# Kernel tuning notes

Hardware: AMD Instinct MI355X
Metric: run time of the kernel (lower is better)

The kernel has to match this reference:

```python
import jax, jax.numpy as jnp
import numpy as np

B, C, D, H, W = 4, 128, 16, 16, 16
INNER = 64  # channels // reduction


def setup_inputs() -> dict:
    key = jax.random.key(0)
    ks = jax.random.split(key, 4)
    s = 0.02
    return {
        "x": jax.random.normal(ks[0], (B, C, D, H, W), dtype=jnp.float32),
        "Wq": jax.random.normal(ks[1], (INNER, C), dtype=jnp.float32) * s,
        "bq": jnp.zeros((INNER,), dtype=jnp.float32),
        "Wk": jax.random.normal(ks[2], (INNER, C), dtype=jnp.float32) * s,
        "bk": jnp.zeros((INNER,), dtype=jnp.float32),
        "Wv": jax.random.normal(ks[3], (C, C), dtype=jnp.float32) * s,
        "bv": jnp.zeros((C,), dtype=jnp.float32),
        "gamma": jnp.zeros((1,), dtype=jnp.float32),
    }


def reference(x, Wq, bq, Wk, bk, Wv, bv, gamma):
    b, c, d, h, w = x.shape
    n = d * h * w
    inner = Wq.shape[0]
    scale = inner ** (-0.5)
    xf = x.reshape(b, c, n)  # flatten spatial dims
    # 1x1 Conv3d == per-position channel matmul
    q = jnp.einsum('oc,bcn->bon', Wq, xf) + bq[None, :, None]  # [B, inner, N]
    k = jnp.einsum('oc,bcn->bon', Wk, xf) + bk[None, :, None]  # [B, inner, N]
    v = jnp.einsum('oc,bcn->bon', Wv, xf) + bv[None, :, None]  # [B, C, N]
    # attn[b, n, m] = softmax_m(q[:, :, n] . k[:, :, m] * scale)
    attn = jax.nn.softmax(jnp.einsum('bon,bom->bnm', q, k) * scale, axis=-1)
    # out = v @ attn^T  -> out[b, c, n] = sum_m v[b, c, m] * attn[b, n, m]
    out = jnp.einsum('bcm,bnm->bcn', v, attn).reshape(b, c, d, h, w)
    return x + gamma[0] * out
```

## Files before the change

kernel.cpp:

```cpp
#include <hip/hip_runtime.h>
#include <cstdint>

#define B_ 4
#define C_ 128
#define INNER_ 64
#define N_ 4096
#define S_ 8
#define KEYS_PER_BLOCK (N_ / S_)
#define KT 64
#define NT (KEYS_PER_BLOCK / KT)

typedef __attribute__((ext_vector_type(8))) short short8;
typedef __attribute__((ext_vector_type(4))) short bf16x4;
typedef __attribute__((ext_vector_type(4))) float f32x4;

typedef const __attribute__((address_space(1))) void* gp_t;
typedef __attribute__((address_space(3))) void* lp_t;

__device__ __forceinline__ short f2bf(float f) {
  unsigned u = __builtin_bit_cast(unsigned, f);
  unsigned r = (u + 0x7FFFu + ((u >> 16) & 1u)) >> 16;
  return (short)r;
}
__device__ __forceinline__ float bf2f(short s) {
  return __builtin_bit_cast(float, ((unsigned)(unsigned short)s) << 16);
}

__device__ __forceinline__ f32x4 mfma16(bf16x4 a, bf16x4 b, f32x4 c) {
#if __has_builtin(__builtin_amdgcn_mfma_f32_16x16x16bf16_1k)
  return __builtin_amdgcn_mfma_f32_16x16x16bf16_1k(a, b, c, 0, 0, 0);
#elif __has_builtin(__builtin_amdgcn_mfma_f32_16x16x16_bf16)
  return __builtin_amdgcn_mfma_f32_16x16x16_bf16(a, b, c, 0, 0, 0);
#else
  f32x4 d;
  asm volatile("v_mfma_f32_16x16x16_bf16 %0, %1, %2, %3"
               : "=v"(d) : "v"(a), "v"(b), "v"(c));
  return d;
#endif
}

__global__ __launch_bounds__(256) void pack_kernel(
    const float* __restrict__ Wq, const float* __restrict__ bq,
    const float* __restrict__ Wk, const float* __restrict__ bk,
    const float* __restrict__ Wv, const float* __restrict__ bv,
    short* __restrict__ wp, float* __restrict__ bp)
{
  const int idx = blockIdx.x * 256 + threadIdx.x;
  const int o = idx >> 7, c = idx & 127;
  float v;
  if (o < 64)       v = Wq[o * C_ + c];
  else if (o < 128) v = Wk[(o - 64) * C_ + c];
  else              v = Wv[(o - 128) * C_ + c];
  wp[idx] = f2bf(v);
  if (c == 0)
    bp[o] = (o < 64) ? bq[o] : (o < 128) ? bk[o - 64] : bv[o - 128];
}

__global__ __launch_bounds__(256) void qkv_kernel(
    const float* __restrict__ x, const short* __restrict__ wp,
    const float* __restrict__ bp,
    short* __restrict__ qg, short* __restrict__ kg, short* __restrict__ vg)
{
  __shared__ short xT[32 * 136];
  __shared__ short outb[256 * 40];
  __shared__ float biasL[256];

  const int tid = threadIdx.x;
  const int b   = blockIdx.x >> 7;
  const int n0  = (blockIdx.x & 127) << 5;

  biasL[tid] = bp[tid];
  const float* xb = x + (size_t)b * C_ * N_ + n0;
  for (int i = tid; i < 1024; i += 256) {
    const int c = i >> 3, seg = i & 7;
    const float4 v = *(const float4*)&xb[(size_t)c * N_ + seg * 4];
    xT[(seg * 4 + 0) * 136 + c] = f2bf(v.x);
    xT[(seg * 4 + 1) * 136 + c] = f2bf(v.y);
    xT[(seg * 4 + 2) * 136 + c] = f2bf(v.z);
    xT[(seg * 4 + 3) * 136 + c] = f2bf(v.w);
  }
  __syncthreads();

  const int w = tid >> 6, lane = tid & 63, quad = lane >> 4, l16 = lane & 15;

  short8 xf[2][4];
#pragma unroll
  for (int nt = 0; nt < 2; ++nt)
#pragma unroll
    for (int kk = 0; kk < 4; ++kk)
      xf[nt][kk] = *(const short8*)&xT[(nt * 16 + l16) * 136 + kk * 32 + quad * 8];

  if (w < 2) {
    const int obase = w * 64;
#pragma unroll
    for (int ot = 0; ot < 4; ++ot) {
      const int o = obase + ot * 16 + l16;
      short8 wf[4];
#pragma unroll
      for (int kk = 0; kk < 4; ++kk)
        wf[kk] = *(const short8*)&wp[(size_t)o * 128 + kk * 32 + quad * 8];
      const float bias = biasL[o];
#pragma unroll
      for (int nt = 0; nt < 2; ++nt) {
        f32x4 acc = (f32x4){0.f, 0.f, 0.f, 0.f};
#pragma unroll
        for (int kk = 0; kk < 4; ++kk)
          acc = __builtin_amdgcn_mfma_f32_16x16x32_bf16(xf[nt][kk], wf[kk], acc, 0, 0, 0);
#pragma unroll
        for (int r = 0; r < 4; ++r)
          outb[o * 40 + nt * 16 + quad * 4 + r] = f2bf(acc[r] + bias);
      }
    }
  } else {
    const int ob2 = (w - 2) * 64;
#pragma unroll
    for (int ot = 0; ot < 4; ++ot) {
      const int orow = 128 + ob2 + ot * 16 + l16;
      short8 wf[4];
#pragma unroll
      for (int kk = 0; kk < 4; ++kk)
        wf[kk] = *(const short8*)&wp[(size_t)orow * 128 + kk * 32 + quad * 8];
#pragma unroll
      for (int nt = 0; nt < 2; ++nt) {
        f32x4 acc = (f32x4){0.f, 0.f, 0.f, 0.f};
#pragma unroll
        for (int kk = 0; kk < 4; ++kk)
          acc = __builtin_amdgcn_mfma_f32_16x16x32_bf16(wf[kk], xf[nt][kk], acc, 0, 0, 0);
#pragma unroll
        for (int r = 0; r < 4; ++r) {
          const int o_r = 128 + ob2 + ot * 16 + quad * 4 + r;
          outb[o_r * 40 + nt * 16 + l16] = f2bf(acc[r] + biasL[o_r]);
        }
      }
    }
  }
  __syncthreads();

  {
    const int n = tid >> 3, oc = tid & 7;
    short8 qv, kv;
#pragma unroll
    for (int j = 0; j < 8; ++j) {
      qv[j] = outb[(oc * 8 + j) * 40 + n];
      kv[j] = outb[(64 + oc * 8 + j) * 40 + n];
    }
    *(short8*)&qg[(((size_t)b * N_ + n0 + n) << 6) + oc * 8] = qv;
    *(short8*)&kg[(((size_t)b * N_ + n0 + n) << 6) + oc * 8] = kv;
#pragma unroll
    for (int rep = 0; rep < 2; ++rep) {
      const int idx2 = tid + rep * 256;
      const int orel = idx2 >> 2, nc = idx2 & 3;
      const short8 vv = *(const short8*)&outb[(128 + orel) * 40 + nc * 8];
      *(short8*)&vg[(((size_t)b * C_ + orel) << 12) + n0 + nc * 8] = vv;
    }
  }
}

__global__ __launch_bounds__(256, 3) void attn_kernel(
    const short* __restrict__ qb, const short* __restrict__ kb,
    const short* __restrict__ vb,
    short* __restrict__ Opart, float* __restrict__ lbuf)
{
  __shared__ short kbuf[2][4096];
  __shared__ short vbuf[2][8192];

  const int tid = threadIdx.x;
  const int bid = blockIdx.x;
  const int b   = bid >> 8;
  const int qt  = (bid >> 3) & 31;
  const int s   = bid & 7;
  const int m0  = qt << 7;
  const int w   = tid >> 6, lane = tid & 63, quad = lane >> 4, l16 = lane & 15;
  const int rbase = m0 + w * 32;

  const float kS = 0.125f * 1.44269504088896340736f;

  short8 qa[2][2];
#pragma unroll
  for (int mt = 0; mt < 2; ++mt)
#pragma unroll
    for (int kk = 0; kk < 2; ++kk)
      qa[mt][kk] = *(const short8*)&qb[((size_t)b * N_ + rbase + mt * 16 + l16) * 64 + kk * 32 + quad * 8];

  float lsum[2] = {0.f, 0.f};
  f32x4 accO[8][2];
#pragma unroll
  for (int vt = 0; vt < 8; ++vt)
#pragma unroll
    for (int mt = 0; mt < 2; ++mt) accO[vt][mt] = (f32x4){0.f, 0.f, 0.f, 0.f};

  const int kslice = s * KEYS_PER_BLOCK;

  auto dma_tile = [&](int kt, int d) {
    const int kbase = kslice + kt * KT;
#pragma unroll
    for (int t = 0; t < 2; ++t) {
      const int p = (w * 2 + t) * 64 + lane;
      const int key = p >> 3, jm = (p & 7) ^ (key & 7);
      const short* src = kb + (((size_t)b * N_ + kbase + key) << 6) + jm * 8;
      __builtin_amdgcn_global_load_lds((gp_t)src, (lp_t)&kbuf[d][(w * 2 + t) * 512], 16, 0, 0);
    }
#pragma unroll
    for (int t = 0; t < 4; ++t) {
      const int p = (w * 4 + t) * 64 + lane;
      const int ch = p >> 3, jm = (p & 7) ^ (ch & 7);
      const short* src = vb + ((size_t)b * C_ + ch) * N_ + kbase + jm * 8;
      __builtin_amdgcn_global_load_lds((gp_t)src, (lp_t)&vbuf[d][(w * 4 + t) * 512], 16, 0, 0);
    }
  };

  dma_tile(0, 0);

  for (int kt = 0; kt < NT; ++kt) {
    __syncthreads();
    if (kt + 1 < NT) dma_tile(kt + 1, (kt + 1) & 1);
    const int d = kt & 1;

    bf16x4 pbf[4][2];
#pragma unroll
    for (int ct = 0; ct < 4; ++ct) {
      const short8 kf0 = *(const short8*)&kbuf[d][((ct * 16 + l16) << 6) + ((quad ^ (l16 & 7)) << 3)];
      const short8 kf1 = *(const short8*)&kbuf[d][((ct * 16 + l16) << 6) + (((4 + quad) ^ (l16 & 7)) << 3)];
#pragma unroll
      for (int mt = 0; mt < 2; ++mt) {
        f32x4 st = (f32x4){0.f, 0.f, 0.f, 0.f};
        st = __builtin_amdgcn_mfma_f32_16x16x32_bf16(kf0, qa[mt][0], st, 0, 0, 0);
        st = __builtin_amdgcn_mfma_f32_16x16x32_bf16(kf1, qa[mt][1], st, 0, 0, 0);
        bf16x4 p4;
#pragma unroll
        for (int r = 0; r < 4; ++r) {
          const float p = exp2f(st[r] * kS);
          lsum[mt] += p;
          p4[r] = f2bf(p);
        }
        pbf[ct][mt] = p4;
      }
    }

#pragma unroll
    for (int vt = 0; vt < 8; ++vt) {
#pragma unroll
      for (int ct = 0; ct < 4; ++ct) {
        const int chunk = ct * 2 + (quad >> 1);
        const bf16x4 vf = *(const bf16x4*)&vbuf[d][((vt * 16 + l16) << 6) +
                              ((chunk ^ (l16 & 7)) << 3) + ((quad & 1) << 2)];
        accO[vt][0] = mfma16(vf, pbf[ct][0], accO[vt][0]);
        accO[vt][1] = mfma16(vf, pbf[ct][1], accO[vt][1]);
      }
    }
  }

#pragma unroll
  for (int mt = 0; mt < 2; ++mt) {
    lsum[mt] += __shfl_xor(lsum[mt], 16);
    lsum[mt] += __shfl_xor(lsum[mt], 32);
  }
  if (quad == 0) {
#pragma unroll
    for (int mt = 0; mt < 2; ++mt)
      lbuf[((size_t)b * S_ + s) * N_ + rbase + mt * 16 + l16] = lsum[mt];
  }
#pragma unroll
  for (int vt = 0; vt < 8; ++vt) {
#pragma unroll
    for (int mt = 0; mt < 2; ++mt) {
#pragma unroll
      for (int r = 0; r < 4; ++r) {
        const int ch = vt * 16 + quad * 4 + r;
        Opart[(((size_t)b * S_ + s) * C_ + ch) * N_ + rbase + mt * 16 + l16] =
            f2bf(accO[vt][mt][r]);
      }
    }
  }
}

__global__ __launch_bounds__(256) void linv_kernel(
    const float* __restrict__ lbuf, float* __restrict__ linv)
{
  const int idx = blockIdx.x * 256 + threadIdx.x;
  const int b = idx >> 12, n = idx & (N_ - 1);
  float L = 0.f;
#pragma unroll
  for (int s = 0; s < S_; ++s) L += lbuf[((size_t)b * S_ + s) * N_ + n];
  linv[idx] = 1.f / L;
}

__global__ __launch_bounds__(256) void combine_kernel(
    const float* __restrict__ x, const float* __restrict__ gamma,
    const short* __restrict__ Opart, const float* __restrict__ linv,
    float* __restrict__ out)
{
  const int idx = blockIdx.x * 256 + threadIdx.x;
  const int n = (idx & 511) << 3;
  const int c = (idx >> 9) & 127;
  const int b = idx >> 16;

  float acc[8];
#pragma unroll
  for (int j = 0; j < 8; ++j) acc[j] = 0.f;
#pragma unroll
  for (int s = 0; s < S_; ++s) {
    const short8 o8 = *(const short8*)&Opart[(((size_t)b * S_ + s) * C_ + c) * N_ + n];
#pragma unroll
    for (int j = 0; j < 8; ++j) acc[j] += bf2f(o8[j]);
  }
  const float4 li0 = *(const float4*)&linv[((size_t)b << 12) + n];
  const float4 li1 = *(const float4*)&linv[((size_t)b << 12) + n + 4];
  const float g = gamma[0];
  const size_t xi = ((size_t)b * C_ + c) * N_ + n;
  const float4 x0 = *(const float4*)&x[xi];
  const float4 x1 = *(const float4*)&x[xi + 4];
  float4 o0, o1;
  o0.x = x0.x + g * acc[0] * li0.x;  o0.y = x0.y + g * acc[1] * li0.y;
  o0.z = x0.z + g * acc[2] * li0.z;  o0.w = x0.w + g * acc[3] * li0.w;
  o1.x = x1.x + g * acc[4] * li1.x;  o1.y = x1.y + g * acc[5] * li1.y;
  o1.z = x1.z + g * acc[6] * li1.z;  o1.w = x1.w + g * acc[7] * li1.w;
  *(float4*)&out[xi] = o0;
  *(float4*)&out[xi + 4] = o1;
}

extern "C" void kernel_launch(void* const* d_in, const int* in_sizes, int n_in,
                              void* d_out, int out_size, void* d_ws, size_t ws_size,
                              hipStream_t stream) {
  const float* x     = (const float*)d_in[0];
  const float* Wq    = (const float*)d_in[1];
  const float* bq    = (const float*)d_in[2];
  const float* Wk    = (const float*)d_in[3];
  const float* bk    = (const float*)d_in[4];
  const float* Wv    = (const float*)d_in[5];
  const float* bv    = (const float*)d_in[6];
  const float* gamma = (const float*)d_in[7];
  float* out = (float*)d_out;

  short* qb = (short*)d_ws;
  short* kb = qb + (size_t)B_ * N_ * INNER_;
  short* vb = kb + (size_t)B_ * N_ * INNER_;
  short* Opart = vb + (size_t)B_ * C_ * N_;
  float* lbuf  = (float*)(Opart + (size_t)B_ * S_ * C_ * N_);
  float* linv  = lbuf + (size_t)B_ * S_ * N_;
  float* bp    = linv + (size_t)B_ * N_;
  short* wp    = (short*)(bp + 256);

  pack_kernel<<<128, 256, 0, stream>>>(Wq, bq, Wk, bk, Wv, bv, wp, bp);
  qkv_kernel<<<B_ * (N_ / 32), 256, 0, stream>>>(x, wp, bp, qb, kb, vb);
  attn_kernel<<<B_ * (N_ / 128) * S_, 256, 0, stream>>>(qb, kb, vb, Opart, lbuf);
  linv_kernel<<<(B_ * N_) / 256, 256, 0, stream>>>(lbuf, linv);
  combine_kernel<<<(B_ * C_ * N_ / 8) / 256, 256, 0, stream>>>(x, gamma, Opart, linv, out);
}
```

Measured before the change: 134.9 us.

## Halve attention key tile to raise occupancy and use packed bf16 conversion

Shrinks the key tile from 64 to 32 keys. This halves the shared K/V double buffers and raises the launch-bounds occupancy hint from 3 to 4 blocks per CU. The V swizzle and DMA mapping are reworked for the narrower tile, and the P-times-V loop order is changed. Probabilities are converted to bf16 with a packed hardware conversion when one is available. The trade-off is twice as many barrier-separated iterations, with less latency hiding per iteration.

```diff
diff --git a/kernel.cpp b/kernel.cpp
--- a/kernel.cpp
+++ b/kernel.cpp
@@ -7,12 +7,13 @@
 #define N_ 4096
 #define S_ 8
 #define KEYS_PER_BLOCK (N_ / S_)
-#define KT 64
+#define KT 32
 #define NT (KEYS_PER_BLOCK / KT)
 
 typedef __attribute__((ext_vector_type(8))) short short8;
 typedef __attribute__((ext_vector_type(4))) short bf16x4;
 typedef __attribute__((ext_vector_type(4))) float f32x4;
+typedef __attribute__((ext_vector_type(2))) unsigned u32x2;
 
 typedef const __attribute__((address_space(1))) void* gp_t;
 typedef __attribute__((address_space(3))) void* lp_t;
@@ -24,6 +25,15 @@
 }
 __device__ __forceinline__ float bf2f(short s) {
   return __builtin_bit_cast(float, ((unsigned)(unsigned short)s) << 16);
+}
+__device__ __forceinline__ unsigned pk2(float lo, float hi) {
+#if __has_builtin(__builtin_amdgcn_cvt_pk_bf16_f32)
+  typedef __attribute__((ext_vector_type(2))) __bf16 bfp;
+  bfp v = __builtin_amdgcn_cvt_pk_bf16_f32(lo, hi);
+  return __builtin_bit_cast(unsigned, v);
+#else
+  return (unsigned)(unsigned short)f2bf(lo) | ((unsigned)(unsigned short)f2bf(hi) << 16);
+#endif
 }
 
 __device__ __forceinline__ f32x4 mfma16(bf16x4 a, bf16x4 b, f32x4 c) {
@@ -156,13 +166,13 @@
   }
 }
 
-__global__ __launch_bounds__(256, 3) void attn_kernel(
+__global__ __launch_bounds__(256, 4) void attn_kernel(
     const short* __restrict__ qb, const short* __restrict__ kb,
     const short* __restrict__ vb,
     short* __restrict__ Opart, float* __restrict__ lbuf)
 {
-  __shared__ short kbuf[2][4096];
-  __shared__ short vbuf[2][8192];
+  __shared__ short kbuf[2][2048];
+  __shared__ short vbuf[2][4096];
 
   const int tid = threadIdx.x;
   const int bid = blockIdx.x;
@@ -193,19 +203,18 @@
 
   auto dma_tile = [&](int kt, int d) {
     const int kbase = kslice + kt * KT;
+    {
+      const int p = w * 64 + lane;
+      const int key = p >> 3, jm = (p & 7) ^ (key & 7);
+      const short* src = kb + (((size_t)b * N_ + kbase + key) << 6) + jm * 8;
+      __builtin_amdgcn_global_load_lds((gp_t)src, (lp_t)&kbuf[d][w * 512], 16, 0, 0);
+    }
 #pragma unroll
     for (int t = 0; t < 2; ++t) {
       const int p = (w * 2 + t) * 64 + lane;
-      const int key = p >> 3, jm = (p & 7) ^ (key & 7);
-      const short* src = kb + (((size_t)b * N_ + kbase + key) << 6) + jm * 8;
-      __builtin_amdgcn_global_load_lds((gp_t)src, (lp_t)&kbuf[d][(w * 2 + t) * 512], 16, 0, 0);
-    }
-#pragma unroll
-    for (int t = 0; t < 4; ++t) {
-      const int p = (w * 4 + t) * 64 + lane;
-      const int ch = p >> 3, jm = (p & 7) ^ (ch & 7);
+      const int ch = p >> 2, jm = (p & 3) ^ (ch & 3);
       const short* src = vb + ((size_t)b * C_ + ch) * N_ + kbase + jm * 8;
-      __builtin_amdgcn_global_load_lds((gp_t)src, (lp_t)&vbuf[d][(w * 4 + t) * 512], 16, 0, 0);
+      __builtin_amdgcn_global_load_lds((gp_t)src, (lp_t)&vbuf[d][(w * 2 + t) * 512], 16, 0, 0);
     }
   };
 
@@ -216,9 +225,9 @@
     if (kt + 1 < NT) dma_tile(kt + 1, (kt + 1) & 1);
     const int d = kt & 1;
 
-    bf16x4 pbf[4][2];
-#pragma unroll
-    for (int ct = 0; ct < 4; ++ct) {
+    bf16x4 pbf[2][2];
+#pragma unroll
+    for (int ct = 0; ct < 2; ++ct) {
       const short8 kf0 = *(const short8*)&kbuf[d][((ct * 16 + l16) << 6) + ((quad ^ (l16 & 7)) << 3)];
       const short8 kf1 = *(const short8*)&kbuf[d][((ct * 16 + l16) << 6) + (((4 + quad) ^ (l16 & 7)) << 3)];
 #pragma unroll
@@ -226,26 +235,26 @@
         f32x4 st = (f32x4){0.f, 0.f, 0.f, 0.f};
         st = __builtin_amdgcn_mfma_f32_16x16x32_bf16(kf0, qa[mt][0], st, 0, 0, 0);
         st = __builtin_amdgcn_mfma_f32_16x16x32_bf16(kf1, qa[mt][1], st, 0, 0, 0);
-        bf16x4 p4;
-#pragma unroll
-        for (int r = 0; r < 4; ++r) {
-          const float p = exp2f(st[r] * kS);
-          lsum[mt] += p;
-          p4[r] = f2bf(p);
-        }
-        pbf[ct][mt] = p4;
-      }
-    }
-
-#pragma unroll
-    for (int vt = 0; vt < 8; ++vt) {
-#pragma unroll
-      for (int ct = 0; ct < 4; ++ct) {
-        const int chunk = ct * 2 + (quad >> 1);
-        const bf16x4 vf = *(const bf16x4*)&vbuf[d][((vt * 16 + l16) << 6) +
-                              ((chunk ^ (l16 & 7)) << 3) + ((quad & 1) << 2)];
-        accO[vt][0] = mfma16(vf, pbf[ct][0], accO[vt][0]);
-        accO[vt][1] = mfma16(vf, pbf[ct][1], accO[vt][1]);
+        const float p0 = exp2f(st[0] * kS);
+        const float p1 = exp2f(st[1] * kS);
+        const float p2 = exp2f(st[2] * kS);
+        const float p3 = exp2f(st[3] * kS);
+        lsum[mt] += (p0 + p1) + (p2 + p3);
+        u32x2 pp;
+        pp[0] = pk2(p0, p1);
+        pp[1] = pk2(p2, p3);
+        pbf[ct][mt] = __builtin_bit_cast(bf16x4, pp);
+      }
+    }
+
+#pragma unroll
+    for (int ks = 0; ks < 2; ++ks) {
+#pragma unroll
+      for (int vt = 0; vt < 8; ++vt) {
+        const bf16x4 vf = *(const bf16x4*)&vbuf[d][((vt * 16 + l16) << 5) +
+                              ((((ks * 2 + (quad >> 1)) ^ (l16 & 3))) << 3) + ((quad & 1) << 2)];
+        accO[vt][0] = mfma16(vf, pbf[ks][0], accO[vt][0]);
+        accO[vt][1] = mfma16(vf, pbf[ks][1], accO[vt][1]);
       }
     }
   }
```

Result: slower. 140.5 us (+4.2%).

## Retile V into MFMA-ready key tiles, rebalance splits, fuse linv into combine

Applied to the files above, without the earlier changes.

The qkv kernel now writes V in a tiled layout (per 64-key tile, grouped in 4-key chunks across channels), so each attention tile DMA is one contiguous copy and V fragments are read from LDS with simple strided loads and no swizzle. The key dimension is split 6 ways instead of 8, giving uneven tile counts per split, which cuts grid size to 768 blocks and shrinks the partial-output buffer. The linv kernel is folded into combine, which computes the reciprocal row sums in shared memory per 64-column block. Softmax probabilities are packed with a paired bf16 convert. The uneven splits create some load imbalance, and the new combine launches fewer blocks, each doing more work.

```diff
diff --git a/kernel.cpp b/kernel.cpp
--- a/kernel.cpp
+++ b/kernel.cpp
@@ -5,14 +5,13 @@
 #define C_ 128
 #define INNER_ 64
 #define N_ 4096
-#define S_ 8
-#define KEYS_PER_BLOCK (N_ / S_)
+#define SPLITS 6
 #define KT 64
-#define NT (KEYS_PER_BLOCK / KT)
 
 typedef __attribute__((ext_vector_type(8))) short short8;
 typedef __attribute__((ext_vector_type(4))) short bf16x4;
 typedef __attribute__((ext_vector_type(4))) float f32x4;
+typedef __attribute__((ext_vector_type(2))) unsigned u32x2;
 
 typedef const __attribute__((address_space(1))) void* gp_t;
 typedef __attribute__((address_space(3))) void* lp_t;
@@ -24,6 +23,15 @@
 }
 __device__ __forceinline__ float bf2f(short s) {
   return __builtin_bit_cast(float, ((unsigned)(unsigned short)s) << 16);
+}
+__device__ __forceinline__ unsigned pk2(float lo, float hi) {
+#if __has_builtin(__builtin_amdgcn_cvt_pk_bf16_f32)
+  typedef __attribute__((ext_vector_type(2))) __bf16 bfp;
+  bfp v = __builtin_amdgcn_cvt_pk_bf16_f32(lo, hi);
+  return __builtin_bit_cast(unsigned, v);
+#else
+  return (unsigned)(unsigned short)f2bf(lo) | ((unsigned)(unsigned short)f2bf(hi) << 16);
+#endif
 }
 
 __device__ __forceinline__ f32x4 mfma16(bf16x4 a, bf16x4 b, f32x4 c) {
@@ -146,12 +154,22 @@
     }
     *(short8*)&qg[(((size_t)b * N_ + n0 + n) << 6) + oc * 8] = qv;
     *(short8*)&kg[(((size_t)b * N_ + n0 + n) << 6) + oc * 8] = kv;
+  }
+  {
+    const int T = n0 >> 6;
+    const int k4base = (n0 & 63) >> 2;
 #pragma unroll
     for (int rep = 0; rep < 2; ++rep) {
-      const int idx2 = tid + rep * 256;
-      const int orel = idx2 >> 2, nc = idx2 & 3;
-      const short8 vv = *(const short8*)&outb[(128 + orel) * 40 + nc * 8];
-      *(short8*)&vg[(((size_t)b * C_ + orel) << 12) + n0 + nc * 8] = vv;
+      const int idx2 = rep * 256 + tid;
+      const int c0  = idx2 & 63;
+      const int k4l = idx2 >> 6;
+      const bf16x4 lo = *(const bf16x4*)&outb[(128 + 2 * c0) * 40 + k4l * 4];
+      const bf16x4 hi = *(const bf16x4*)&outb[(128 + 2 * c0 + 1) * 40 + k4l * 4];
+      short8 vv;
+#pragma unroll
+      for (int j = 0; j < 4; ++j) { vv[j] = lo[j]; vv[4 + j] = hi[j]; }
+      const size_t tb = (((size_t)b * 64 + T) * 16 + k4base + k4l) * 512 + c0 * 8;
+      *(short8*)&vg[tb] = vv;
     }
   }
 }
@@ -166,13 +184,16 @@
 
   const int tid = threadIdx.x;
   const int bid = blockIdx.x;
-  const int b   = bid >> 8;
-  const int qt  = (bid >> 3) & 31;
-  const int s   = bid & 7;
+  const int s   = bid % 6;
+  const int qt  = (bid / 6) & 31;
+  const int b   = bid / 192;
   const int m0  = qt << 7;
   const int w   = tid >> 6, lane = tid & 63, quad = lane >> 4, l16 = lane & 15;
   const int rbase = m0 + w * 32;
 
+  const int t0  = (s * 64) / 6;
+  const int NTs = ((s + 1) * 64) / 6 - t0;
+
   const float kS = 0.125f * 1.44269504088896340736f;
 
   short8 qa[2][2];
@@ -189,31 +210,29 @@
 #pragma unroll
     for (int mt = 0; mt < 2; ++mt) accO[vt][mt] = (f32x4){0.f, 0.f, 0.f, 0.f};
 
-  const int kslice = s * KEYS_PER_BLOCK;
-
   auto dma_tile = [&](int kt, int d) {
-    const int kbase = kslice + kt * KT;
+    const int T = t0 + kt;
+    const short* kbp = kb + (((size_t)b * N_ + T * 64) << 6);
 #pragma unroll
     for (int t = 0; t < 2; ++t) {
       const int p = (w * 2 + t) * 64 + lane;
       const int key = p >> 3, jm = (p & 7) ^ (key & 7);
-      const short* src = kb + (((size_t)b * N_ + kbase + key) << 6) + jm * 8;
+      const short* src = kbp + (key << 6) + jm * 8;
       __builtin_amdgcn_global_load_lds((gp_t)src, (lp_t)&kbuf[d][(w * 2 + t) * 512], 16, 0, 0);
     }
+    const short* vtp = vb + ((size_t)b * 64 + T) * 8192;
 #pragma unroll
     for (int t = 0; t < 4; ++t) {
       const int p = (w * 4 + t) * 64 + lane;
-      const int ch = p >> 3, jm = (p & 7) ^ (ch & 7);
-      const short* src = vb + ((size_t)b * C_ + ch) * N_ + kbase + jm * 8;
-      __builtin_amdgcn_global_load_lds((gp_t)src, (lp_t)&vbuf[d][(w * 4 + t) * 512], 16, 0, 0);
+      __builtin_amdgcn_global_load_lds((gp_t)(vtp + p * 8), (lp_t)&vbuf[d][(w * 4 + t) * 512], 16, 0, 0);
     }
   };
 
   dma_tile(0, 0);
 
-  for (int kt = 0; kt < NT; ++kt) {
+  for (int kt = 0; kt < NTs; ++kt) {
     __syncthreads();
-    if (kt + 1 < NT) dma_tile(kt + 1, (kt + 1) & 1);
+    if (kt + 1 < NTs) dma_tile(kt + 1, (kt + 1) & 1);
     const int d = kt & 1;
 
     bf16x4 pbf[4][2];
@@ -226,14 +245,15 @@
         f32x4 st = (f32x4){0.f, 0.f, 0.f, 0.f};
         st = __builtin_amdgcn_mfma_f32_16x16x32_bf16(kf0, qa[mt][0], st, 0, 0, 0);
         st = __builtin_amdgcn_mfma_f32_16x16x32_bf16(kf1, qa[mt][1], st, 0, 0, 0);
-        bf16x4 p4;
-#pragma unroll
-        for (int r = 0; r < 4; ++r) {
-          const float p = exp2f(st[r] * kS);
-          lsum[mt] += p;
-          p4[r] = f2bf(p);
-        }
-        pbf[ct][mt] = p4;
+        const float p0 = exp2f(st[0] * kS);
+        const float p1 = exp2f(st[1] * kS);
+        const float p2 = exp2f(st[2] * kS);
+        const float p3 = exp2f(st[3] * kS);
+        lsum[mt] += (p0 + p1) + (p2 + p3);
+        u32x2 pp;
+        pp[0] = pk2(p0, p1);
+        pp[1] = pk2(p2, p3);
+        pbf[ct][mt] = __builtin_bit_cast(bf16x4, pp);
       }
     }
 
@@ -241,9 +261,7 @@
     for (int vt = 0; vt < 8; ++vt) {
 #pragma unroll
       for (int ct = 0; ct < 4; ++ct) {
-        const int chunk = ct * 2 + (quad >> 1);
-        const bf16x4 vf = *(const bf16x4*)&vbuf[d][((vt * 16 + l16) << 6) +
-                              ((chunk ^ (l16 & 7)) << 3) + ((quad & 1) << 2)];
+        const bf16x4 vf = *(const bf16x4*)&vbuf[d][(ct * 4 + quad) * 512 + (vt * 16 + l16) * 4];
         accO[vt][0] = mfma16(vf, pbf[ct][0], accO[vt][0]);
         accO[vt][1] = mfma16(vf, pbf[ct][1], accO[vt][1]);
       }
@@ -258,7 +276,7 @@
   if (quad == 0) {
 #pragma unroll
     for (int mt = 0; mt < 2; ++mt)
-      lbuf[((size_t)b * S_ + s) * N_ + rbase + mt * 16 + l16] = lsum[mt];
+      lbuf[((size_t)b * SPLITS + s) * N_ + rbase + mt * 16 + l16] = lsum[mt];
   }
 #pragma unroll
   for (int vt = 0; vt < 8; ++vt) {
@@ -267,56 +285,52 @@
 #pragma unroll
       for (int r = 0; r < 4; ++r) {
         const int ch = vt * 16 + quad * 4 + r;
-        Opart[(((size_t)b * S_ + s) * C_ + ch) * N_ + rbase + mt * 16 + l16] =
+        Opart[(((size_t)b * SPLITS + s) * C_ + ch) * N_ + rbase + mt * 16 + l16] =
             f2bf(accO[vt][mt][r]);
       }
     }
   }
-}
-
-__global__ __launch_bounds__(256) void linv_kernel(
-    const float* __restrict__ lbuf, float* __restrict__ linv)
-{
-  const int idx = blockIdx.x * 256 + threadIdx.x;
-  const int b = idx >> 12, n = idx & (N_ - 1);
-  float L = 0.f;
-#pragma unroll
-  for (int s = 0; s < S_; ++s) L += lbuf[((size_t)b * S_ + s) * N_ + n];
-  linv[idx] = 1.f / L;
 }
 
 __global__ __launch_bounds__(256) void combine_kernel(
     const float* __restrict__ x, const float* __restrict__ gamma,
-    const short* __restrict__ Opart, const float* __restrict__ linv,
+    const short* __restrict__ Opart, const float* __restrict__ lbuf,
     float* __restrict__ out)
 {
-  const int idx = blockIdx.x * 256 + threadIdx.x;
-  const int n = (idx & 511) << 3;
-  const int c = (idx >> 9) & 127;
-  const int b = idx >> 16;
-
-  float acc[8];
-#pragma unroll
-  for (int j = 0; j < 8; ++j) acc[j] = 0.f;
-#pragma unroll
-  for (int s = 0; s < S_; ++s) {
-    const short8 o8 = *(const short8*)&Opart[(((size_t)b * S_ + s) * C_ + c) * N_ + n];
-#pragma unroll
-    for (int j = 0; j < 8; ++j) acc[j] += bf2f(o8[j]);
-  }
-  const float4 li0 = *(const float4*)&linv[((size_t)b << 12) + n];
-  const float4 li1 = *(const float4*)&linv[((size_t)b << 12) + n + 4];
+  __shared__ float linvL[64];
+  const int tid = threadIdx.x;
+  const int b   = blockIdx.x >> 6;
+  const int n0  = (blockIdx.x & 63) << 6;
+
+  if (tid < 64) {
+    float L = 0.f;
+#pragma unroll
+    for (int s = 0; s < SPLITS; ++s) L += lbuf[((size_t)b * SPLITS + s) * N_ + n0 + tid];
+    linvL[tid] = 1.f / L;
+  }
+  __syncthreads();
+
   const float g = gamma[0];
-  const size_t xi = ((size_t)b * C_ + c) * N_ + n;
-  const float4 x0 = *(const float4*)&x[xi];
-  const float4 x1 = *(const float4*)&x[xi + 4];
-  float4 o0, o1;
-  o0.x = x0.x + g * acc[0] * li0.x;  o0.y = x0.y + g * acc[1] * li0.y;
-  o0.z = x0.z + g * acc[2] * li0.z;  o0.w = x0.w + g * acc[3] * li0.w;
-  o1.x = x1.x + g * acc[4] * li1.x;  o1.y = x1.y + g * acc[5] * li1.y;
-  o1.z = x1.z + g * acc[6] * li1.z;  o1.w = x1.w + g * acc[7] * li1.w;
-  *(float4*)&out[xi] = o0;
-  *(float4*)&out[xi + 4] = o1;
+  const int n4 = (tid & 15) * 4, cb = tid >> 4;
+#pragma unroll
+  for (int cp = 0; cp < 8; ++cp) {
+    const int c = cp * 16 + cb;
+    float acc[4] = {0.f, 0.f, 0.f, 0.f};
+#pragma unroll
+    for (int s = 0; s < SPLITS; ++s) {
+      const bf16x4 o4 = *(const bf16x4*)&Opart[(((size_t)b * SPLITS + s) * C_ + c) * N_ + n0 + n4];
+#pragma unroll
+      for (int j = 0; j < 4; ++j) acc[j] += bf2f(o4[j]);
+    }
+    const size_t xi = ((size_t)b * C_ + c) * N_ + n0 + n4;
+    const float4 xv = *(const float4*)&x[xi];
+    float4 ov;
+    ov.x = xv.x + g * acc[0] * linvL[n4 + 0];
+    ov.y = xv.y + g * acc[1] * linvL[n4 + 1];
+    ov.z = xv.z + g * acc[2] * linvL[n4 + 2];
+    ov.w = xv.w + g * acc[3] * linvL[n4 + 3];
+    *(float4*)&out[xi] = ov;
+  }
 }
 
 extern "C" void kernel_launch(void* const* d_in, const int* in_sizes, int n_in,
@@ -336,14 +350,12 @@
   short* kb = qb + (size_t)B_ * N_ * INNER_;
   short* vb = kb + (size_t)B_ * N_ * INNER_;
   short* Opart = vb + (size_t)B_ * C_ * N_;
-  float* lbuf  = (float*)(Opart + (size_t)B_ * S_ * C_ * N_);
-  float* linv  = lbuf + (size_t)B_ * S_ * N_;
-  float* bp    = linv + (size_t)B_ * N_;
+  float* lbuf  = (float*)(Opart + (size_t)B_ * SPLITS * C_ * N_);
+  float* bp    = lbuf + (size_t)B_ * SPLITS * N_;
   short* wp    = (short*)(bp + 256);
 
   pack_kernel<<<128, 256, 0, stream>>>(Wq, bq, Wk, bk, Wv, bv, wp, bp);
   qkv_kernel<<<B_ * (N_ / 32), 256, 0, stream>>>(x, wp, bp, qb, kb, vb);
-  attn_kernel<<<B_ * (N_ / 128) * S_, 256, 0, stream>>>(qb, kb, vb, Opart, lbuf);
-  linv_kernel<<<(B_ * N_) / 256, 256, 0, stream>>>(lbuf, linv);
-  combine_kernel<<<(B_ * C_ * N_ / 8) / 256, 256, 0, stream>>>(x, gamma, Opart, linv, out);
-}
+  attn_kernel<<<B_ * 32 * SPLITS, 256, 0, stream>>>(qb, kb, vb, Opart, lbuf);
+  combine_kernel<<<B_ * (N_ / 64), 256, 0, stream>>>(x, gamma, Opart, lbuf, out);
+}
```

Result: no change. 134.0 us (-0.6%).
